# Optimization experiments

Hardware: AMD Instinct MI355X
Metric: run time of the kernel (lower is better)

## Reference

```python
import jax, jax.numpy as jnp
import numpy as np

B, T, S, D, H, F = 4, 1024, 1024, 1024, 16, 4096
NEG = jnp.float32(-1e9)


def _ln(x, g, b):
    m = jnp.mean(x, axis=-1, keepdims=True)
    v = jnp.mean((x - m) ** 2, axis=-1, keepdims=True)
    return (x - m) * jax.lax.rsqrt(v + 1e-5) * g + b


def _mha(q, k, v, wq, bq, wk, bk, wv, bv, wo, bo, scale, mask, causal, sbias):
    Bq, Tq, Dq = q.shape
    Sk = k.shape[1]
    dk = Dq // H
    Q = (q @ wq.T + bq).reshape(Bq, Tq, H, dk).transpose(0, 2, 1, 3)  # [B,H,T,dk]
    K = (k @ wk.T + bk).reshape(Bq, Sk, H, dk).transpose(0, 2, 1, 3)  # [B,H,S,dk]
    V = (v @ wv.T + bv).reshape(Bq, Sk, H, dk).transpose(0, 2, 1, 3)
    s = jnp.einsum('bhtd,bhsd->bhts', Q, K) / jnp.sqrt(jnp.float32(dk))
    if sbias is not None:
        s = s + scale * sbias[:, None, None, :]
    if mask is not None:
        s = jnp.where(mask == 0, NEG, s)
    if causal is not None:
        s = jnp.where(causal == 0, NEG, s)
    a = jax.nn.softmax(s, axis=-1)
    o = jnp.einsum('bhts,bhsd->bhtd', a, V).transpose(0, 2, 1, 3).reshape(Bq, Tq, Dq)
    return o @ wo.T + bo


def setup_inputs():
    key = jax.random.key(0)
    ks = jax.random.split(key, 16)
    r = lambda i, shape, s=0.02: jax.random.normal(ks[i], shape, dtype=jnp.float32) * s
    z = lambda *shape: jnp.zeros(shape, jnp.float32)
    o = lambda *shape: jnp.ones(shape, jnp.float32)
    inp = dict(
        x=r(0, (B, T, D), 1.0),
        memory=r(1, (B, S, D), 1.0),
        sentence_bias=r(2, (B, S), 1.0),
        trg_mask=jnp.ones((B, 1, 1, T), jnp.int32),
        trg_causal_mask=jnp.tril(jnp.ones((T, T), jnp.int32))[None, None],
        src_mask=jnp.ones((B, 1, 1, S), jnp.int32),
        sa_wq=r(3, (D, D)), sa_bq=z(D), sa_wk=r(4, (D, D)), sa_bk=z(D),
        sa_wv=r(5, (D, D)), sa_bv=z(D), sa_wo=r(6, (D, D)), sa_bo=z(D),
        sa_scale=jnp.float32(0.1),
        ca_wq=r(7, (D, D)), ca_bq=z(D), ca_wk=r(8, (D, D)), ca_bk=z(D),
        ca_wv=r(9, (D, D)), ca_bv=z(D), ca_wo=r(10, (D, D)), ca_bo=z(D),
        ca_scale=jnp.float32(0.1),
        ln1_g=o(D), ln1_b=z(D), ln2_g=o(D), ln2_b=z(D), ln3_g=o(D), ln3_b=z(D),
        ffn_w1=r(11, (F, D)), ffn_b1=z(F), ffn_w2=r(12, (D, F)), ffn_b2=z(D),
    )
    return inp


def reference(x, memory, trg_mask, trg_causal_mask, src_mask, sentence_bias,
              sa_wq, sa_bq, sa_wk, sa_bk, sa_wv, sa_bv, sa_wo, sa_bo, sa_scale,
              ca_wq, ca_bq, ca_wk, ca_bk, ca_wv, ca_bv, ca_wo, ca_bo, ca_scale,
              ln1_g, ln1_b, ln2_g, ln2_b, ln3_g, ln3_b,
              ffn_w1, ffn_b1, ffn_w2, ffn_b2):
    # Faithful quirk: Q comes from normed x, K/V from raw residual stream.
    x = x + _mha(_ln(x, ln1_g, ln1_b), x, x,
                 sa_wq, sa_bq, sa_wk, sa_bk, sa_wv, sa_bv, sa_wo, sa_bo,
                 sa_scale, trg_mask, trg_causal_mask, None)
    x = x + _mha(_ln(x, ln2_g, ln2_b), memory, memory,
                 ca_wq, ca_bq, ca_wk, ca_bk, ca_wv, ca_bv, ca_wo, ca_bo,
                 ca_scale, src_mask, None, sentence_bias)
    h = _ln(x, ln3_g, ln3_b)
    x = x + (jax.nn.relu(h @ ffn_w1.T + ffn_b1) @ ffn_w2.T + ffn_b2)
    return x
```

## Files before the change

kernel.cpp:

```cpp
#include <hip/hip_runtime.h>
#include <hip/hip_bf16.h>
#include <cmath>
#include <stdint.h>

typedef __hip_bfloat16 bf16;
typedef __attribute__((ext_vector_type(8))) __bf16 bf16x8;
typedef __attribute__((ext_vector_type(8))) unsigned short u16x8;
typedef __attribute__((ext_vector_type(4))) float f32x4;

__device__ __forceinline__ void gld16(const void* g, const void* l)
{
    __builtin_amdgcn_global_load_lds(
        (const __attribute__((address_space(1))) unsigned int*)(unsigned long long)g,
        (__attribute__((address_space(3))) unsigned int*)(unsigned int)(unsigned long long)l,
        16, 0, 0);
}

struct CvtSrcs { const float* p[24]; };

__global__ __launch_bounds__(256) void cvt_all(
    CvtSrcs s, bf16* __restrict__ dst,
    const float* __restrict__ lg, const float* __restrict__ lb,
    bf16* __restrict__ lnout)
{
    const int t = threadIdx.x;
    const int i = (blockIdx.x * 256 + t) * 8;
    const int seg = i >> 20;
    const float* sp = s.p[seg] + (i & 1048575);
    const float4 a = *(const float4*)(sp);
    const float4 b = *(const float4*)(sp + 4);
    const float v[8] = {a.x, a.y, a.z, a.w, b.x, b.y, b.z, b.w};
    bf16 tmp[8];
#pragma unroll
    for (int j = 0; j < 8; ++j) tmp[j] = __float2bfloat16(v[j]);
    *(uint4*)(dst + i) = *(const uint4*)tmp;

    if (seg < 4) {
        float s1 = 0.f, s2 = 0.f;
#pragma unroll
        for (int j = 0; j < 8; ++j) { s1 += v[j]; s2 += v[j] * v[j]; }
#pragma unroll
        for (int off = 32; off > 0; off >>= 1) {
            s1 += __shfl_xor(s1, off, 64);
            s2 += __shfl_xor(s2, off, 64);
        }
        __shared__ float r1[4], r2[4];
        const int w = t >> 6;
        if ((t & 63) == 0) { r1[w] = s1; r2[w] = s2; }
        __syncthreads();
        const int rw = (w >> 1) * 2;
        s1 = r1[rw] + r1[rw + 1];
        s2 = r2[rw] + r2[rw + 1];
        const float mean = s1 * (1.f / 1024.f);
        const float var  = s2 * (1.f / 1024.f) - mean * mean;
        const float rstd = rsqrtf(var + 1e-5f);
        bf16 lt[8];
        const int c0 = i & 1023;
#pragma unroll
        for (int j = 0; j < 8; ++j)
            lt[j] = __float2bfloat16((v[j] - mean) * rstd * lg[c0 + j] + lb[c0 + j]);
        *(uint4*)(lnout + i) = *(const uint4*)lt;
    }
}

enum {
    EPI_QSCALE = 0,
    EPI_KV = 1,
    EPI_RELU = 2,
    EPI_RES_F32_F32OUT = 3,
    EPI_PART = 4
};

template <int EPI>
__global__ __launch_bounds__(512, 2) void gemm256(
    const bf16* __restrict__ A, const bf16* __restrict__ W,
    const float* __restrict__ bias, void* __restrict__ out,
    int N, int Kiter, int Kstride)
{
    __shared__ __align__(16) unsigned short sA[2][2][128 * 64];
    __shared__ __align__(16) unsigned short sB[2][2][128 * 64];

    const int t  = threadIdx.x;
    const int l  = t & 63;
    const int w  = t >> 6;
    const int wv = w * 64;
    const int wr = w >> 2;
    const int wc = w & 3;
    const int lm = l & 15;
    const int kq = l >> 4;
    const int rx = lm & 7;

    int bx = blockIdx.x;
    const int xcd = bx & 7;
    const int ib  = bx >> 3;
    const int bm  = xcd * 2 + (ib & 1);
    const int bn  = ib >> 1;

    const bf16* gA = A + (size_t)(bm * 256 + (t >> 3)) * Kstride
                       + ((t & 7) ^ ((t >> 3) & 7)) * 8;
    const bf16* gB = W + (size_t)(bn * 256 + (t >> 3)) * Kstride
                       + ((t & 7) ^ ((t >> 3) & 7)) * 8;

#define SQA(slot, kt, j)                                        \
    gld16(gA + (size_t)((j) * 64) * Kstride + (kt) * 64,        \
          &sA[slot][(j) >> 1][(((j) & 1) * 512 + wv) * 8])
#define SQB(slot, kt, j)                                        \
    gld16(gB + (size_t)((j) * 64) * Kstride + (kt) * 64,        \
          &sB[slot][(j) >> 1][(((j) & 1) * 512 + wv) * 8])

    bf16x8 af[4][2], bg[2][2];

#define READ_AF(s_, mh)                                                     \
    do {                                                                    \
        _Pragma("unroll")                                                   \
        for (int mi = 0; mi < 4; ++mi)                                      \
            _Pragma("unroll")                                               \
            for (int kk = 0; kk < 2; ++kk) {                                \
                const int lr = (mh) * 64 + mi * 16 + lm;                    \
                const int sl = ((kk << 2) | kq) ^ rx;                       \
                af[mi][kk] = __builtin_bit_cast(bf16x8,                     \
                    *(const u16x8*)(&sA[s_][wr][lr * 64 + sl * 8]));        \
            }                                                               \
    } while (0)
#define READ_BG(s_, nh)                                                     \
    do {                                                                    \
        _Pragma("unroll")                                                   \
        for (int ni = 0; ni < 2; ++ni)                                      \
            _Pragma("unroll")                                               \
            for (int kk = 0; kk < 2; ++kk) {                                \
                const int lr = (wc & 1) * 64 + (nh) * 32 + ni * 16 + lm;    \
                const int sl = ((kk << 2) | kq) ^ rx;                       \
                bg[ni][kk] = __builtin_bit_cast(bf16x8,                     \
                    *(const u16x8*)(&sB[s_][wc >> 1][lr * 64 + sl * 8]));   \
            }                                                               \
    } while (0)
#define MFMA_QUAD(mh, nh)                                                   \
    do {                                                                    \
        __builtin_amdgcn_s_setprio(1);                                      \
        _Pragma("unroll")                                                   \
        for (int mi = 0; mi < 4; ++mi)                                      \
            _Pragma("unroll")                                               \
            for (int ni = 0; ni < 2; ++ni)                                  \
                _Pragma("unroll")                                           \
                for (int kk = 0; kk < 2; ++kk)                              \
                    acc[(mh) * 4 + mi][(nh) * 2 + ni] =                     \
                        __builtin_amdgcn_mfma_f32_16x16x32_bf16(            \
                            af[mi][kk], bg[ni][kk],                         \
                            acc[(mh) * 4 + mi][(nh) * 2 + ni], 0, 0, 0);    \
        __builtin_amdgcn_s_setprio(0);                                      \
    } while (0)
#define BARRIER() do { __builtin_amdgcn_s_barrier();                        \
                       __builtin_amdgcn_sched_barrier(0); } while (0)
#define WAITV2() asm volatile("s_waitcnt vmcnt(2)" ::: "memory")
#define WAITV0() asm volatile("s_waitcnt vmcnt(0)" ::: "memory")

    f32x4 acc[8][4] = {};
    const int NT = Kiter >> 6;

    SQB(0, 0, 0); SQB(0, 0, 1); SQB(0, 0, 2); SQB(0, 0, 3);
    SQA(0, 0, 0); SQA(0, 0, 2); SQA(0, 0, 1); SQA(0, 0, 3);

    for (int tt = 0; tt < NT - 1; ++tt) {
        const int s = tt & 1, d = s ^ 1, kn = tt + 1;
        WAITV2(); BARRIER();
        SQB(d, kn, 0); SQB(d, kn, 1);
        READ_AF(s, 0); READ_BG(s, 0);
        MFMA_QUAD(0, 0);
        WAITV2(); BARRIER();
        SQB(d, kn, 2); SQB(d, kn, 3);
        READ_AF(s, 1);
        MFMA_QUAD(1, 0);
        SQA(d, kn, 0); SQA(d, kn, 2);
        READ_BG(s, 1);
        MFMA_QUAD(1, 1);
        SQA(d, kn, 1); SQA(d, kn, 3);
        READ_AF(s, 0);
        MFMA_QUAD(0, 1);
    }
    {
        const int s = (NT - 1) & 1;
        WAITV2(); BARRIER();
        READ_AF(s, 0); READ_BG(s, 0);
        MFMA_QUAD(0, 0);
        WAITV0(); BARRIER();
        READ_AF(s, 1);
        MFMA_QUAD(1, 0);
        READ_BG(s, 1);
        MFMA_QUAD(1, 1);
        READ_AF(s, 0);
        MFMA_QUAD(0, 1);
    }

    __syncthreads();
    unsigned short* scr = (w < 4) ? &sA[0][0][0] + w * 8192
                                  : &sB[0][0][0] + (w - 4) * 8192;

#pragma unroll
    for (int NI = 0; NI < 4; ++NI) {
        const int col = bn * 256 + wc * 64 + NI * 16 + lm;
        const float bv = bias[col];
        const int c  = NI * 2 + (lm >> 3);
        const int ci = lm & 7;
#pragma unroll
        for (int MI = 0; MI < 8; ++MI) {
#pragma unroll
            for (int r = 0; r < 4; ++r) {
                float v = acc[MI][NI][r] + bv;
                if (EPI == EPI_RELU) v = fmaxf(v, 0.f);
                const int row = MI * 16 + kq * 4 + r;
                scr[row * 64 + ((c ^ (row & 7)) * 8) + ci] =
                    __builtin_bit_cast(unsigned short, (__bf16)v);
            }
        }
    }
#pragma unroll
    for (int it = 0; it < 16; ++it) {
        const int row = it * 8 + (l >> 3);
        const int lc  = l & 7;
        const u16x8 vv = *(const u16x8*)&scr[row * 64 + ((lc ^ (row & 7)) * 8)];
        const int Crow = bm * 256 + wr * 128 + row;
        const int Ccol = bn * 256 + wc * 64 + lc * 8;
        *(u16x8*)((bf16*)out + (size_t)Crow * N + Ccol) = vv;
    }
#undef SQA
#undef SQB
#undef READ_AF
#undef READ_BG
#undef MFMA_QUAD
}

template <int EPI>
__global__ __launch_bounds__(256, 3) void gemm_bt(
    const bf16* __restrict__ A, const bf16* __restrict__ W,
    const float* __restrict__ bias, const float* __restrict__ bias2,
    const float* __restrict__ res, void* __restrict__ out,
    int M, int N, int Kiter, int Kstride)
{
    __shared__ __align__(16) unsigned short sA[2][128 * 64];
    __shared__ __align__(16) unsigned short sB[2][64 * 64];

    const int t  = threadIdx.x;
    const int l  = t & 63;
    const int w  = t >> 6;
    const int wv = w * 64;
    const int wr = w >> 1;
    const int wc = w & 1;
    const int lm = l & 15;
    const int kq = l >> 4;
    const int rx = lm & 7;

    const int bx  = blockIdx.x;
    const int xcd = bx & 7;
    const int ib  = bx >> 3;
    const int bm  = xcd * 4 + (ib & 3);
    const int bn  = ib >> 2;

    const bf16* gA = A + (size_t)(bm * 128 + (t >> 3)) * Kstride
                       + ((t & 7) ^ ((t >> 3) & 7)) * 8;
    const bf16* gB = W + (size_t)(bn * 64 + (t >> 3)) * Kstride
                       + ((t & 7) ^ ((t >> 3) & 7)) * 8;

#define SQA(slot, kt, j)                                        \
    gld16(gA + (size_t)((j) * 32) * Kstride + (kt) * 64,        \
          &sA[slot][((j) * 256 + wv) * 8])
#define SQB(slot, kt, j)                                        \
    gld16(gB + (size_t)((j) * 32) * Kstride + (kt) * 64,        \
          &sB[slot][((j) * 256 + wv) * 8])

    bf16x8 af[4][2], bg[2][2];

#define READ_A(s_, mh, kk)                                                  \
    do {                                                                    \
        _Pragma("unroll")                                                   \
        for (int m2 = 0; m2 < 2; ++m2) {                                    \
            const int mi = (mh) * 2 + m2;                                   \
            const int lr = wr * 64 + mi * 16 + lm;                          \
            const int sl = (((kk) << 2) | kq) ^ rx;                         \
            af[mi][kk] = __builtin_bit_cast(bf16x8,                         \
                *(const u16x8*)(&sA[s_][lr * 64 + sl * 8]));                \
        }                                                                   \
    } while (0)
#define READ_B(s_, kk)                                                      \
    do {                                                                    \
        _Pragma("unroll")                                                   \
        for (int ni = 0; ni < 2; ++ni) {                                    \
            const int lr = wc * 32 + ni * 16 + lm;                          \
            const int sl = (((kk) << 2) | kq) ^ rx;                         \
            bg[ni][kk] = __builtin_bit_cast(bf16x8,                         \
                *(const u16x8*)(&sB[s_][lr * 64 + sl * 8]));                \
        }                                                                   \
    } while (0)
#define MFMA_PH(mh, kk)                                                     \
    do {                                                                    \
        __builtin_amdgcn_s_setprio(1);                                      \
        _Pragma("unroll")                                                   \
        for (int m2 = 0; m2 < 2; ++m2)                                      \
            _Pragma("unroll")                                               \
            for (int ni = 0; ni < 2; ++ni)                                  \
                acc[(mh) * 2 + m2][ni] =                                    \
                    __builtin_amdgcn_mfma_f32_16x16x32_bf16(                \
                        af[(mh) * 2 + m2][kk], bg[ni][kk],                  \
                        acc[(mh) * 2 + m2][ni], 0, 0, 0);                   \
        __builtin_amdgcn_s_setprio(0);                                      \
    } while (0)
#define BARRIER() do { __builtin_amdgcn_s_barrier();                        \
                       __builtin_amdgcn_sched_barrier(0); } while (0)
#define WAITV2() asm volatile("s_waitcnt vmcnt(2)" ::: "memory")
#define WAITV0() asm volatile("s_waitcnt vmcnt(0)" ::: "memory")

    f32x4 acc[4][2] = {};
    const int NT = Kiter >> 6;

    SQB(0, 0, 0); SQB(0, 0, 1);
    SQA(0, 0, 0); SQA(0, 0, 2);
    SQA(0, 0, 1); SQA(0, 0, 3);

    for (int tt = 0; tt < NT - 1; ++tt) {
        const int s = tt & 1, d = s ^ 1, kn = tt + 1;
        WAITV2(); BARRIER();
        SQB(d, kn, 0); SQB(d, kn, 1);
        READ_A(s, 0, 0); READ_B(s, 0);
        MFMA_PH(0, 0);
        WAITV2(); BARRIER();
        SQA(d, kn, 0); SQA(d, kn, 2);
        READ_A(s, 1, 0);
        MFMA_PH(1, 0);
        SQA(d, kn, 1); SQA(d, kn, 3);
        READ_A(s, 1, 1); READ_B(s, 1);
        MFMA_PH(1, 1);
        READ_A(s, 0, 1);
        MFMA_PH(0, 1);
    }
    {
        const int s = (NT - 1) & 1;
        WAITV2(); BARRIER();
        READ_A(s, 0, 0); READ_B(s, 0);
        MFMA_PH(0, 0);
        WAITV0(); BARRIER();
        READ_A(s, 1, 0);
        MFMA_PH(1, 0);
        READ_A(s, 1, 1); READ_B(s, 1);
        MFMA_PH(1, 1);
        READ_A(s, 0, 1);
        MFMA_PH(0, 1);
    }
#undef SQA
#undef SQB
#undef READ_A
#undef READ_B
#undef MFMA_PH
#undef BARRIER
#undef WAITV2
#undef WAITV0

#pragma unroll
    for (int ni = 0; ni < 2; ++ni) {
        const int col = bn * 64 + wc * 32 + ni * 16 + lm;
        float bv = 0.f;
        if (EPI == EPI_KV) bv = (col < 1024) ? bias[col] : bias2[col - 1024];
        else bv = bias[col];
#pragma unroll
        for (int mi = 0; mi < 4; ++mi) {
#pragma unroll
            for (int r = 0; r < 4; ++r) {
                const int row = bm * 128 + wr * 64 + mi * 16 + kq * 4 + r;
                float v = acc[mi][ni][r] + bv;
                if (EPI == EPI_QSCALE) v *= 0.125f;
                if (EPI == EPI_KV) {
                    if (col < 1024) {
                        ((bf16*)out)[(size_t)row * 1024 + col] = __float2bfloat16(v);
                    } else {
                        const int ch = col - 1024;
                        const size_t idx = (size_t)4 * 1048576 +
                            ((size_t)((row >> 10) * 16 + (ch >> 6)) * 64 + (ch & 63)) * 1024
                            + (row & 1023);
                        ((bf16*)out)[idx] = __float2bfloat16(v);
                    }
                } else if (EPI == EPI_RES_F32_F32OUT) {
                    const size_t idx = (size_t)row * N + col;
                    ((float*)out)[idx] = v + res[idx];
                } else {
                    ((bf16*)out)[(size_t)row * N + col] = __float2bfloat16(v);
                }
            }
        }
    }
}

template <bool CAUSAL, bool SBIAS>
__global__ __launch_bounds__(256, 2) void flash_attn(
    const bf16* __restrict__ Q, const bf16* __restrict__ K,
    const bf16* __restrict__ Vt, bf16* __restrict__ O,
    const float* __restrict__ sbias, const float* __restrict__ scale_ptr)
{
    __shared__ __align__(16) unsigned short sK[2][64 * 64];
    __shared__ __align__(16) unsigned short sV[2][64 * 64];
    __shared__ __align__(16) unsigned short sP[4 * 32 * 72];

    const int t  = threadIdx.x;
    const int l  = t & 63;
    const int w  = t >> 6;
    const int wv = w * 64;
    const int lm = l & 15;
    const int kq = l >> 4;

    const int bh = blockIdx.x & 63;
    const int qb = blockIdx.x >> 6;
    const int h  = bh & 15;
    const int b  = bh >> 4;

    const int tb = qb * 128 + w * 32;
    const size_t qrow0 = (size_t)(b * 1024 + tb) * 1024 + h * 64;

    bf16x8 qf[2][2];
#pragma unroll
    for (int mi = 0; mi < 2; ++mi)
#pragma unroll
        for (int kk = 0; kk < 2; ++kk)
            qf[mi][kk] = __builtin_bit_cast(bf16x8,
                *(const u16x8*)(Q + qrow0 + (size_t)(mi * 16 + lm) * 1024 + kk * 32 + kq * 8));

    float cs = 0.f; const float* sb = nullptr;
    if (SBIAS) { cs = scale_ptr[0]; sb = sbias + b * 1024; }

    const bf16* gK = K  + (size_t)(b * 1024 + (t >> 3)) * 1024 + h * 64
                   + ((t & 7) ^ ((t >> 3) & 7)) * 8;
    const bf16* gV = Vt + (size_t)((b * 16 + h) * 64 + (t >> 3)) * 1024
                   + ((t & 7) ^ ((t >> 3) & 7)) * 8;
    __bf16* sPw = (__bf16*)sP + w * 32 * 72;

#define STAGE_KV(buf, s0r)                                                   \
    do {                                                                     \
        gld16(gK + (size_t)(s0r) * 1024,        &sK[buf][wv * 8]);           \
        gld16(gK + (size_t)((s0r) + 32) * 1024, &sK[buf][2048 + wv * 8]);    \
        gld16(gV + (s0r),                       &sV[buf][wv * 8]);           \
        gld16(gV + (s0r) + 32 * 1024,           &sV[buf][2048 + wv * 8]);    \
    } while (0)

    const int niter = CAUSAL ? (2 * qb + 2) : 16;

    STAGE_KV(0, 0);
    __syncthreads();

    f32x4 acc_o[2][4] = {};
    f32x4 l_run[2] = {};

    for (int it = 0; it < niter; ++it) {
        const int s0 = it * 64;
        const int cur = it & 1;

        if (it + 1 < niter) STAGE_KV(cur ^ 1, s0 + 64);

        f32x4 accs[2][4] = {};
#pragma unroll
        for (int ni = 0; ni < 4; ++ni)
#pragma unroll
            for (int kk = 0; kk < 2; ++kk) {
                const bf16x8 kf = __builtin_bit_cast(bf16x8,
                    *(const u16x8*)(&sK[cur][(ni * 16 + lm) * 64
                        + ((((kk << 2) | kq)) ^ (lm & 7)) * 8]));
#pragma unroll
                for (int mi = 0; mi < 2; ++mi)
                    accs[mi][ni] = __builtin_amdgcn_mfma_f32_16x16x32_bf16(
                        qf[mi][kk], kf, accs[mi][ni], 0, 0, 0);
            }

        if (SBIAS) {
#pragma unroll
            for (int ni = 0; ni < 4; ++ni) {
                const float sv = cs * sb[s0 + ni * 16 + lm];
#pragma unroll
                for (int mi = 0; mi < 2; ++mi)
#pragma unroll
                    for (int r = 0; r < 4; ++r) accs[mi][ni][r] += sv;
            }
        }
        if (CAUSAL && (s0 + 63 > tb)) {
#pragma unroll
            for (int ni = 0; ni < 4; ++ni) {
                const int s = s0 + ni * 16 + lm;
#pragma unroll
                for (int mi = 0; mi < 2; ++mi)
#pragma unroll
                    for (int r = 0; r < 4; ++r)
                        if (s > tb + mi * 16 + kq * 4 + r) accs[mi][ni][r] = -1e30f;
            }
        }

#pragma unroll
        for (int mi = 0; mi < 2; ++mi)
#pragma unroll
            for (int ni = 0; ni < 4; ++ni)
#pragma unroll
                for (int r = 0; r < 4; ++r) {
                    const float e = __expf(accs[mi][ni][r]);
                    l_run[mi][r] += e;
                    sPw[(mi * 16 + kq * 4 + r) * 72 + ni * 16 + lm] = (__bf16)e;
                }

#pragma unroll
        for (int kk = 0; kk < 2; ++kk) {
            bf16x8 pf[2];
#pragma unroll
            for (int mi = 0; mi < 2; ++mi)
                pf[mi] = __builtin_bit_cast(bf16x8,
                    *(const u16x8*)(sPw + (mi * 16 + lm) * 72 + kk * 32 + kq * 8));
#pragma unroll
            for (int di = 0; di < 4; ++di) {
                const bf16x8 vf = __builtin_bit_cast(bf16x8,
                    *(const u16x8*)(&sV[cur][(di * 16 + lm) * 64
                        + ((((kk << 2) | kq)) ^ (lm & 7)) * 8]));
#pragma unroll
                for (int mi = 0; mi < 2; ++mi)
                    acc_o[mi][di] = __builtin_amdgcn_mfma_f32_16x16x32_bf16(
                        pf[mi], vf, acc_o[mi][di], 0, 0, 0);
            }
        }

        __syncthreads();
    }
#undef STAGE_KV

#pragma unroll
    for (int mi = 0; mi < 2; ++mi) {
        f32x4 lt = l_run[mi];
#pragma unroll
        for (int x = 1; x < 16; x <<= 1)
#pragma unroll
            for (int r = 0; r < 4; ++r) lt[r] += __shfl_xor(lt[r], x, 64);
#pragma unroll
        for (int r = 0; r < 4; ++r) lt[r] = 1.f / lt[r];
#pragma unroll
        for (int di = 0; di < 4; ++di)
#pragma unroll
            for (int r = 0; r < 4; ++r) {
                const size_t idx = (size_t)(b * 1024 + tb + mi * 16 + kq * 4 + r) * 1024
                                 + h * 64 + di * 16 + lm;
                O[idx] = __float2bfloat16(acc_o[mi][di][r] * lt[r]);
            }
    }
}

__global__ __launch_bounds__(256) void ln_kernel(
    const float* __restrict__ xin, const float* __restrict__ g,
    const float* __restrict__ bta, bf16* __restrict__ out)
{
    const int row = blockIdx.x;
    const int t = threadIdx.x;
    const size_t base = (size_t)row * 1024 + t * 4;

    const float4 f = *(const float4*)(xin + base);
    const float v[4] = {f.x, f.y, f.z, f.w};
    float s1 = v[0] + v[1] + v[2] + v[3];
    float s2 = v[0]*v[0] + v[1]*v[1] + v[2]*v[2] + v[3]*v[3];
#pragma unroll
    for (int off = 32; off > 0; off >>= 1) {
        s1 += __shfl_xor(s1, off, 64);
        s2 += __shfl_xor(s2, off, 64);
    }
    __shared__ float r1[4], r2[4];
    if ((t & 63) == 0) { r1[t >> 6] = s1; r2[t >> 6] = s2; }
    __syncthreads();
    s1 = r1[0] + r1[1] + r1[2] + r1[3];
    s2 = r2[0] + r2[1] + r2[2] + r2[3];
    const float mean = s1 * (1.f / 1024.f);
    const float var  = s2 * (1.f / 1024.f) - mean * mean;
    const float rstd = rsqrtf(var + 1e-5f);
#pragma unroll
    for (int j = 0; j < 4; ++j) {
        const int c = t * 4 + j;
        out[base + j] = __float2bfloat16((v[j] - mean) * rstd * g[c] + bta[c]);
    }
}

extern "C" void kernel_launch(void* const* d_in, const int* in_sizes, int n_in,
                              void* d_out, int out_size, void* d_ws, size_t ws_size,
                              hipStream_t stream)
{
    const float* x       = (const float*)d_in[0];
    const float* memory  = (const float*)d_in[1];
    const float* sbias   = (const float*)d_in[2];
    const float* sa_bq = (const float*)d_in[7];
    const float* sa_bk = (const float*)d_in[9];
    const float* sa_bv = (const float*)d_in[11];
    const float* sa_bo = (const float*)d_in[13];
    const float* ca_bq = (const float*)d_in[16];
    const float* ca_bk = (const float*)d_in[18];
    const float* ca_bv = (const float*)d_in[20];
    const float* ca_bo = (const float*)d_in[22];
    const float* ca_scale = (const float*)d_in[23];
    const float* ln1_g = (const float*)d_in[24]; const float* ln1_b = (const float*)d_in[25];
    const float* ln2_g = (const float*)d_in[26]; const float* ln2_b = (const float*)d_in[27];
    const float* ln3_g = (const float*)d_in[28]; const float* ln3_b = (const float*)d_in[29];
    const float* b1 = (const float*)d_in[31];
    const float* b2 = (const float*)d_in[33];

    char* ws = (char*)d_ws;
    const size_t MB = (size_t)1 << 20;
    float* x1    = (float*)(ws + 0 * MB);
    float* x2    = (float*)(ws + 16 * MB);
    bf16* lnbuf  = (bf16*)(ws + 32 * MB);
    bf16* Qb     = (bf16*)(ws + 40 * MB);
    bf16* Kb     = (bf16*)(ws + 48 * MB);
    bf16* Vtb    = (bf16*)(ws + 56 * MB);
    bf16* Ob     = (bf16*)(ws + 64 * MB);
    bf16* ffnmid = (bf16*)(ws + 40 * MB);
    bf16* wx     = (bf16*)(ws + 72 * MB);
    bf16* wmem   = (bf16*)(ws + 80 * MB);
    bf16* bw     = (bf16*)(ws + 88 * MB);
    bf16* b_sa_wq = bw + 0 * 1048576, *b_sa_wk = bw + 1 * 1048576;
    bf16* b_sa_wo = bw + 3 * 1048576;
    bf16* b_ca_wq = bw + 4 * 1048576, *b_ca_wk = bw + 5 * 1048576;
    bf16* b_ca_wo = bw + 7 * 1048576;
    bf16* b_w1   = (bf16*)(ws + 104 * MB);
    bf16* b_w2   = (bf16*)(ws + 112 * MB);

    const int M = 4096;
    dim3 blk256(256), blk512(512);
    const dim3 gQ(512);
    const dim3 gKV(1024);
    const dim3 gFA(512);
    const dim3 g256(256);

    CvtSrcs cs;
    for (int c = 0; c < 4; ++c) {
        cs.p[c]      = x + (size_t)c * 1048576;
        cs.p[4 + c]  = memory + (size_t)c * 1048576;
        cs.p[16 + c] = (const float*)d_in[30] + (size_t)c * 1048576;
        cs.p[20 + c] = (const float*)d_in[32] + (size_t)c * 1048576;
    }
    cs.p[8]  = (const float*)d_in[6];
    cs.p[9]  = (const float*)d_in[8];
    cs.p[10] = (const float*)d_in[10];
    cs.p[11] = (const float*)d_in[12];
    cs.p[12] = (const float*)d_in[15];
    cs.p[13] = (const float*)d_in[17];
    cs.p[14] = (const float*)d_in[19];
    cs.p[15] = (const float*)d_in[21];
    cvt_all<<<24 * 1048576 / 2048, blk256, 0, stream>>>(
        cs, wx, ln1_g, ln1_b, lnbuf);

    gemm_bt<EPI_QSCALE><<<gQ, blk256, 0, stream>>>(
        lnbuf, b_sa_wq, sa_bq, nullptr, nullptr, Qb, M, 1024, 1024, 1024);
    gemm_bt<EPI_KV><<<gKV, blk256, 0, stream>>>(
        wx, b_sa_wk, sa_bk, sa_bv, nullptr, Kb, M, 2048, 1024, 1024);
    flash_attn<true, false><<<gFA, blk256, 0, stream>>>(Qb, Kb, Vtb, Ob, nullptr, nullptr);
    gemm_bt<EPI_RES_F32_F32OUT><<<gQ, blk256, 0, stream>>>(
        Ob, b_sa_wo, sa_bo, nullptr, x, x1, M, 1024, 1024, 1024);

    ln_kernel<<<4096, blk256, 0, stream>>>(x1, ln2_g, ln2_b, lnbuf);
    gemm_bt<EPI_QSCALE><<<gQ, blk256, 0, stream>>>(
        lnbuf, b_ca_wq, ca_bq, nullptr, nullptr, Qb, M, 1024, 1024, 1024);
    gemm_bt<EPI_KV><<<gKV, blk256, 0, stream>>>(
        wmem, b_ca_wk, ca_bk, ca_bv, nullptr, Kb, M, 2048, 1024, 1024);
    flash_attn<false, true><<<gFA, blk256, 0, stream>>>(Qb, Kb, Vtb, Ob, sbias, ca_scale);
    gemm_bt<EPI_RES_F32_F32OUT><<<gQ, blk256, 0, stream>>>(
        Ob, b_ca_wo, ca_bo, nullptr, x1, x2, M, 1024, 1024, 1024);

    ln_kernel<<<4096, blk256, 0, stream>>>(x2, ln3_g, ln3_b, lnbuf);
    gemm256<EPI_RELU><<<g256, blk512, 0, stream>>>(
        lnbuf, b_w1, b1, ffnmid, 4096, 1024, 1024);
    gemm_bt<EPI_RES_F32_F32OUT><<<gQ, blk256, 0, stream>>>(
        ffnmid, b_w2, b2, nullptr, x2, d_out, M, 1024, 4096, 4096);
}
```

Baseline: 457.3 us.

## Merge Q and KV projection launches and reschedule gemm256 LDS/barrier pipeline

```diff
diff --git a/kernel.cpp b/kernel.cpp
--- a/kernel.cpp
+++ b/kernel.cpp
@@ -151,6 +151,8 @@
     } while (0)
 #define BARRIER() do { __builtin_amdgcn_s_barrier();                        \
                        __builtin_amdgcn_sched_barrier(0); } while (0)
+#define LGKM0() do { asm volatile("s_waitcnt lgkmcnt(0)" ::: "memory");     \
+                     __builtin_amdgcn_sched_barrier(0); } while (0)
 #define WAITV2() asm volatile("s_waitcnt vmcnt(2)" ::: "memory")
 #define WAITV0() asm volatile("s_waitcnt vmcnt(0)" ::: "memory")
 
@@ -159,30 +161,41 @@
 
     SQB(0, 0, 0); SQB(0, 0, 1); SQB(0, 0, 2); SQB(0, 0, 3);
     SQA(0, 0, 0); SQA(0, 0, 2); SQA(0, 0, 1); SQA(0, 0, 3);
+    WAITV2();
+    __syncthreads();
 
     for (int tt = 0; tt < NT - 1; ++tt) {
         const int s = tt & 1, d = s ^ 1, kn = tt + 1;
-        WAITV2(); BARRIER();
+        READ_AF(s, 0); READ_BG(s, 0);
         SQB(d, kn, 0); SQB(d, kn, 1);
-        READ_AF(s, 0); READ_BG(s, 0);
+        WAITV2();
+        BARRIER(); LGKM0();
         MFMA_QUAD(0, 0);
-        WAITV2(); BARRIER();
+        BARRIER();
+        READ_AF(s, 1);
         SQB(d, kn, 2); SQB(d, kn, 3);
-        READ_AF(s, 1);
+        BARRIER(); LGKM0();
         MFMA_QUAD(1, 0);
+        BARRIER();
+        READ_BG(s, 1);
         SQA(d, kn, 0); SQA(d, kn, 2);
-        READ_BG(s, 1);
+        BARRIER(); LGKM0();
         MFMA_QUAD(1, 1);
+        BARRIER();
+        READ_AF(s, 0);
         SQA(d, kn, 1); SQA(d, kn, 3);
-        READ_AF(s, 0);
+        WAITV2();
+        BARRIER(); LGKM0();
         MFMA_QUAD(0, 1);
+        BARRIER();
     }
     {
         const int s = (NT - 1) & 1;
-        WAITV2(); BARRIER();
         READ_AF(s, 0); READ_BG(s, 0);
+        WAITV0();
+        BARRIER(); LGKM0();
         MFMA_QUAD(0, 0);
-        WAITV0(); BARRIER();
+        BARRIER();
         READ_AF(s, 1);
         MFMA_QUAD(1, 0);
         READ_BG(s, 1);
@@ -227,18 +240,20 @@
 #undef READ_AF
 #undef READ_BG
 #undef MFMA_QUAD
+#undef BARRIER
+#undef LGKM0
+#undef WAITV2
+#undef WAITV0
 }
 
 template <int EPI>
-__global__ __launch_bounds__(256, 3) void gemm_bt(
+__device__ __forceinline__ void gemm_bt_body(
+    unsigned short* __restrict__ sAp, unsigned short* __restrict__ sBp,
     const bf16* __restrict__ A, const bf16* __restrict__ W,
     const float* __restrict__ bias, const float* __restrict__ bias2,
     const float* __restrict__ res, void* __restrict__ out,
-    int M, int N, int Kiter, int Kstride)
-{
-    __shared__ __align__(16) unsigned short sA[2][128 * 64];
-    __shared__ __align__(16) unsigned short sB[2][64 * 64];
-
+    int N, int Kiter, int Kstride, int bx)
+{
     const int t  = threadIdx.x;
     const int l  = t & 63;
     const int w  = t >> 6;
@@ -249,7 +264,6 @@
     const int kq = l >> 4;
     const int rx = lm & 7;
 
-    const int bx  = blockIdx.x;
     const int xcd = bx & 7;
     const int ib  = bx >> 3;
     const int bm  = xcd * 4 + (ib & 3);
@@ -260,16 +274,16 @@
     const bf16* gB = W + (size_t)(bn * 64 + (t >> 3)) * Kstride
                        + ((t & 7) ^ ((t >> 3) & 7)) * 8;
 
-#define SQA(slot, kt, j)                                        \
+#define SQA_B(slot, kt, j)                                      \
     gld16(gA + (size_t)((j) * 32) * Kstride + (kt) * 64,        \
-          &sA[slot][((j) * 256 + wv) * 8])
-#define SQB(slot, kt, j)                                        \
+          sAp + (slot) * 8192 + ((j) * 256 + wv) * 8)
+#define SQB_B(slot, kt, j)                                      \
     gld16(gB + (size_t)((j) * 32) * Kstride + (kt) * 64,        \
-          &sB[slot][((j) * 256 + wv) * 8])
+          sBp + (slot) * 4096 + ((j) * 256 + wv) * 8)
 
     bf16x8 af[4][2], bg[2][2];
 
-#define READ_A(s_, mh, kk)                                                  \
+#define READ_A_B(s_, mh, kk)                                                \
     do {                                                                    \
         _Pragma("unroll")                                                   \
         for (int m2 = 0; m2 < 2; ++m2) {                                    \
@@ -277,20 +291,20 @@
             const int lr = wr * 64 + mi * 16 + lm;                          \
             const int sl = (((kk) << 2) | kq) ^ rx;                         \
             af[mi][kk] = __builtin_bit_cast(bf16x8,                         \
-                *(const u16x8*)(&sA[s_][lr * 64 + sl * 8]));                \
+                *(const u16x8*)(sAp + (s_) * 8192 + lr * 64 + sl * 8));     \
         }                                                                   \
     } while (0)
-#define READ_B(s_, kk)                                                      \
+#define READ_B_B(s_, kk)                                                    \
     do {                                                                    \
         _Pragma("unroll")                                                   \
         for (int ni = 0; ni < 2; ++ni) {                                    \
             const int lr = wc * 32 + ni * 16 + lm;                          \
             const int sl = (((kk) << 2) | kq) ^ rx;                         \
             bg[ni][kk] = __builtin_bit_cast(bf16x8,                         \
-                *(const u16x8*)(&sB[s_][lr * 64 + sl * 8]));                \
+                *(const u16x8*)(sBp + (s_) * 4096 + lr * 64 + sl * 8));     \
         }                                                                   \
     } while (0)
-#define MFMA_PH(mh, kk)                                                     \
+#define MFMA_PH_B(mh, kk)                                                   \
     do {                                                                    \
         __builtin_amdgcn_s_setprio(1);                                      \
         _Pragma("unroll")                                                   \
@@ -303,55 +317,55 @@
                         acc[(mh) * 2 + m2][ni], 0, 0, 0);                   \
         __builtin_amdgcn_s_setprio(0);                                      \
     } while (0)
-#define BARRIER() do { __builtin_amdgcn_s_barrier();                        \
-                       __builtin_amdgcn_sched_barrier(0); } while (0)
-#define WAITV2() asm volatile("s_waitcnt vmcnt(2)" ::: "memory")
-#define WAITV0() asm volatile("s_waitcnt vmcnt(0)" ::: "memory")
+#define BARRIER_B() do { __builtin_amdgcn_s_barrier();                      \
+                         __builtin_amdgcn_sched_barrier(0); } while (0)
+#define WAITV2_B() asm volatile("s_waitcnt vmcnt(2)" ::: "memory")
+#define WAITV0_B() asm volatile("s_waitcnt vmcnt(0)" ::: "memory")
 
     f32x4 acc[4][2] = {};
     const int NT = Kiter >> 6;
 
-    SQB(0, 0, 0); SQB(0, 0, 1);
-    SQA(0, 0, 0); SQA(0, 0, 2);
-    SQA(0, 0, 1); SQA(0, 0, 3);
+    SQB_B(0, 0, 0); SQB_B(0, 0, 1);
+    SQA_B(0, 0, 0); SQA_B(0, 0, 2);
+    SQA_B(0, 0, 1); SQA_B(0, 0, 3);
 
     for (int tt = 0; tt < NT - 1; ++tt) {
         const int s = tt & 1, d = s ^ 1, kn = tt + 1;
-        WAITV2(); BARRIER();
-        SQB(d, kn, 0); SQB(d, kn, 1);
-        READ_A(s, 0, 0); READ_B(s, 0);
-        MFMA_PH(0, 0);
-        WAITV2(); BARRIER();
-        SQA(d, kn, 0); SQA(d, kn, 2);
-        READ_A(s, 1, 0);
-        MFMA_PH(1, 0);
-        SQA(d, kn, 1); SQA(d, kn, 3);
-        READ_A(s, 1, 1); READ_B(s, 1);
-        MFMA_PH(1, 1);
-        READ_A(s, 0, 1);
-        MFMA_PH(0, 1);
+        WAITV2_B(); BARRIER_B();
+        SQB_B(d, kn, 0); SQB_B(d, kn, 1);
+        READ_A_B(s, 0, 0); READ_B_B(s, 0);
+        MFMA_PH_B(0, 0);
+        WAITV2_B(); BARRIER_B();
+        SQA_B(d, kn, 0); SQA_B(d, kn, 2);
+        READ_A_B(s, 1, 0);
+        MFMA_PH_B(1, 0);
+        SQA_B(d, kn, 1); SQA_B(d, kn, 3);
+        READ_A_B(s, 1, 1); READ_B_B(s, 1);
+        MFMA_PH_B(1, 1);
+        READ_A_B(s, 0, 1);
+        MFMA_PH_B(0, 1);
     }
     {
         const int s = (NT - 1) & 1;
-        WAITV2(); BARRIER();
-        READ_A(s, 0, 0); READ_B(s, 0);
-        MFMA_PH(0, 0);
-        WAITV0(); BARRIER();
-        READ_A(s, 1, 0);
-        MFMA_PH(1, 0);
-        READ_A(s, 1, 1); READ_B(s, 1);
-        MFMA_PH(1, 1);
-        READ_A(s, 0, 1);
-        MFMA_PH(0, 1);
-    }
-#undef SQA
-#undef SQB
-#undef READ_A
-#undef READ_B
-#undef MFMA_PH
-#undef BARRIER
-#undef WAITV2
-#undef WAITV0
+        WAITV2_B(); BARRIER_B();
+        READ_A_B(s, 0, 0); READ_B_B(s, 0);
+        MFMA_PH_B(0, 0);
+        WAITV0_B(); BARRIER_B();
+        READ_A_B(s, 1, 0);
+        MFMA_PH_B(1, 0);
+        READ_A_B(s, 1, 1); READ_B_B(s, 1);
+        MFMA_PH_B(1, 1);
+        READ_A_B(s, 0, 1);
+        MFMA_PH_B(0, 1);
+    }
+#undef SQA_B
+#undef SQB_B
+#undef READ_A_B
+#undef READ_B_B
+#undef MFMA_PH_B
+#undef BARRIER_B
+#undef WAITV2_B
+#undef WAITV0_B
 
 #pragma unroll
     for (int ni = 0; ni < 2; ++ni) {
@@ -366,6 +380,7 @@
                 const int row = bm * 128 + wr * 64 + mi * 16 + kq * 4 + r;
                 float v = acc[mi][ni][r] + bv;
                 if (EPI == EPI_QSCALE) v *= 0.125f;
+                if (EPI == EPI_RELU) v = fmaxf(v, 0.f);
                 if (EPI == EPI_KV) {
                     if (col < 1024) {
                         ((bf16*)out)[(size_t)row * 1024 + col] = __float2bfloat16(v);
@@ -385,6 +400,37 @@
             }
         }
     }
+}
+
+template <int EPI>
+__global__ __launch_bounds__(256, 3) void gemm_bt(
+    const bf16* __restrict__ A, const bf16* __restrict__ W,
+    const float* __restrict__ bias, const float* __restrict__ bias2,
+    const float* __restrict__ res, void* __restrict__ out,
+    int M, int N, int Kiter, int Kstride)
+{
+    __shared__ __align__(16) unsigned short sA[2 * 128 * 64];
+    __shared__ __align__(16) unsigned short sB[2 * 64 * 64];
+    gemm_bt_body<EPI>(sA, sB, A, W, bias, bias2, res, out,
+                      N, Kiter, Kstride, blockIdx.x);
+}
+
+__global__ __launch_bounds__(256, 3) void qkv_fused(
+    const bf16* __restrict__ Aq, const bf16* __restrict__ Wq,
+    const float* __restrict__ bq, bf16* __restrict__ Qb,
+    const bf16* __restrict__ Akv, const bf16* __restrict__ Wkv,
+    const float* __restrict__ bk, const float* __restrict__ bv,
+    bf16* __restrict__ Kb)
+{
+    __shared__ __align__(16) unsigned short sA[2 * 128 * 64];
+    __shared__ __align__(16) unsigned short sB[2 * 64 * 64];
+    const int bx = blockIdx.x;
+    if (bx < 512)
+        gemm_bt_body<EPI_QSCALE>(sA, sB, Aq, Wq, bq, nullptr, nullptr, Qb,
+                                 1024, 1024, 1024, bx);
+    else
+        gemm_bt_body<EPI_KV>(sA, sB, Akv, Wkv, bk, bv, nullptr, Kb,
+                             2048, 1024, 1024, bx - 512);
 }
 
 template <bool CAUSAL, bool SBIAS>
@@ -618,7 +664,7 @@
     const int M = 4096;
     dim3 blk256(256), blk512(512);
     const dim3 gQ(512);
-    const dim3 gKV(1024);
+    const dim3 gQKV(1536);
     const dim3 gFA(512);
     const dim3 g256(256);
 
@@ -640,19 +686,15 @@
     cvt_all<<<24 * 1048576 / 2048, blk256, 0, stream>>>(
         cs, wx, ln1_g, ln1_b, lnbuf);
 
-    gemm_bt<EPI_QSCALE><<<gQ, blk256, 0, stream>>>(
-        lnbuf, b_sa_wq, sa_bq, nullptr, nullptr, Qb, M, 1024, 1024, 1024);
-    gemm_bt<EPI_KV><<<gKV, blk256, 0, stream>>>(
-        wx, b_sa_wk, sa_bk, sa_bv, nullptr, Kb, M, 2048, 1024, 1024);
+    qkv_fused<<<gQKV, blk256, 0, stream>>>(
+        lnbuf, b_sa_wq, sa_bq, Qb, wx, b_sa_wk, sa_bk, sa_bv, Kb);
     flash_attn<true, false><<<gFA, blk256, 0, stream>>>(Qb, Kb, Vtb, Ob, nullptr, nullptr);
     gemm_bt<EPI_RES_F32_F32OUT><<<gQ, blk256, 0, stream>>>(
         Ob, b_sa_wo, sa_bo, nullptr, x, x1, M, 1024, 1024, 1024);
 
     ln_kernel<<<4096, blk256, 0, stream>>>(x1, ln2_g, ln2_b, lnbuf);
-    gemm_bt<EPI_QSCALE><<<gQ, blk256, 0, stream>>>(
-        lnbuf, b_ca_wq, ca_bq, nullptr, nullptr, Qb, M, 1024, 1024, 1024);
-    gemm_bt<EPI_KV><<<gKV, blk256, 0, stream>>>(
-        wmem, b_ca_wk, ca_bk, ca_bv, nullptr, Kb, M, 2048, 1024, 1024);
+    qkv_fused<<<gQKV, blk256, 0, stream>>>(
+        lnbuf, b_ca_wq, ca_bq, Qb, wmem, b_ca_wk, ca_bk, ca_bv, Kb);
     flash_attn<false, true><<<gFA, blk256, 0, stream>>>(Qb, Kb, Vtb, Ob, sbias, ca_scale);
     gemm_bt<EPI_RES_F32_F32OUT><<<gQ, blk256, 0, stream>>>(
         Ob, b_ca_wo, ca_bo, nullptr, x1, x2, M, 1024, 1024, 1024);
```

After: 460.4 us. No clear change (+0.7%).
